# Kernel optimization log

Measured on AMD Instinct MI355X. Metric: run time of the kernel, lower is better.

Reference implementation:

```python
import jax, jax.numpy as jnp
import numpy as np

B, M, N = 32, 2048, 2048
W_PRIMAL, W_DUAL, W_STAT, W_COMP = 0.1, 0.1, 0.6, 0.2


def setup_inputs() -> dict:
    key = jax.random.key(0)
    k1, k2, k3, k4, k5 = jax.random.split(key, 5)
    return {
        "x_hat": jax.random.normal(k1, (B * N,), dtype=jnp.float32),
        "lam_hat": jax.random.normal(k2, (B * M,), dtype=jnp.float32),
        "A": jax.random.normal(k3, (B, M, N), dtype=jnp.float32),
        "b_pad": jax.random.normal(k4, (B, M), dtype=jnp.float32),
        "c_pad": jax.random.normal(k5, (B, N), dtype=jnp.float32),
        "b_mask": jnp.ones((B, M), dtype=bool),
        "c_mask": jnp.ones((B, N), dtype=bool),
    }


def reference(x_hat, lam_hat, A, b_pad, c_pad, b_mask, c_mask):
    # Uniform sizes: x_hat is the concatenation of B vectors of length N,
    # lam_hat of B vectors of length M. b_mask/c_mask are unused by the
    # original forward (full padding assumed here).
    b, m, n = A.shape
    x = x_hat.reshape(b, n)
    lam = lam_hat.reshape(b, m)

    # Batched mat-vec products (the spmm calls in the original, fp32 math).
    Ax_minus_b = jnp.einsum("bmn,bn->bm", A, x) - b_pad        # [B, M]
    At_lambda = jnp.einsum("bmn,bm->bn", A, lam)               # [B, N]

    # Per-sample mean, summed over batch, then * (1/B) == global mean
    # (sizes are uniform).
    loss_primal = jnp.mean(jnp.square(jax.nn.relu(Ax_minus_b)))
    loss_dual = jnp.mean(jnp.square(jax.nn.relu(-lam)))
    loss_stat = jnp.mean(jnp.square(At_lambda + c_pad))
    loss_comp = jnp.mean(jnp.square(lam * Ax_minus_b))

    total = (W_PRIMAL * loss_primal + W_DUAL * loss_dual
             + W_STAT * loss_stat + W_COMP * loss_comp)
    return total
```

## Files before the change

kernel.cpp:

```cpp
#include <hip/hip_runtime.h>

#define BB 32
#define MM 2048
#define NN 2048
#define ROWS 64
#define CHUNKS (MM / ROWS)
#define THREADS 256

typedef float f32x4 __attribute__((ext_vector_type(4)));

#define P0 ((size_t)BB * CHUNKS * NN)
#define P1 (P0 + 2 * BB * CHUNKS)
#define FIN_BLOCKS 64

__device__ __forceinline__ float waveReduceSum(float v) {
#pragma unroll
    for (int off = 32; off > 0; off >>= 1)
        v += __shfl_down(v, off, 64);
    return v;
}

__global__ __launch_bounds__(THREADS) void fused_main(
    const float* __restrict__ x_hat, const float* __restrict__ lam_hat,
    const float* __restrict__ A, const float* __restrict__ b_pad,
    float* __restrict__ ws) {
    const int b = blockIdx.y;
    const int chunk = blockIdx.x;
    const int m0 = chunk * ROWS;
    const int t = threadIdx.x;
    const int wave = t >> 6;
    const int lane = t & 63;

    __shared__ float lamS[ROWS];
    __shared__ float wp[ROWS * 4];

    if (t < ROWS) lamS[t] = lam_hat[b * MM + m0 + t];
    __syncthreads();

    const f32x4* xv = (const f32x4*)(x_hat + (size_t)b * NN);
    const f32x4 x0 = xv[t];
    const f32x4 x1 = xv[256 + t];

    f32x4 at0 = (f32x4)(0.f);
    f32x4 at1 = (f32x4)(0.f);

    const f32x4* Ab = (const f32x4*)(A + ((size_t)b * MM + (size_t)m0) * NN);

    for (int r = 0; r < ROWS; ++r) {
        const f32x4* ap = Ab + (size_t)r * (NN / 4);
        f32x4 a0 = __builtin_nontemporal_load(ap + t);
        f32x4 a1 = __builtin_nontemporal_load(ap + 256 + t);
        float lm = lamS[r];
        f32x4 d = a0 * x0 + a1 * x1;
        float dot = d.x + d.y + d.z + d.w;
        at0 += a0 * lm;
        at1 += a1 * lm;
        float wsum = waveReduceSum(dot);
        if (lane == 0) wp[r * 4 + wave] = wsum;
    }
    __syncthreads();

    if (t < ROWS) {
        int r = t;
        float y = wp[r * 4 + 0] + wp[r * 4 + 1] + wp[r * 4 + 2] + wp[r * 4 + 3]
                - b_pad[b * MM + m0 + r];
        float lm = lamS[r];
        float ry = fmaxf(y, 0.f);
        float pr = ry * ry;
        float cm = lm * y;
        cm = cm * cm;
        pr = waveReduceSum(pr);
        cm = waveReduceSum(cm);
        if (t == 0) {
            float* prcm = ws + P0 + ((size_t)b * CHUNKS + chunk) * 2;
            prcm[0] = pr;
            prcm[1] = cm;
        }
    }

    f32x4* dst = (f32x4*)(ws + ((size_t)b * CHUNKS + chunk) * NN);
    dst[t] = at0;
    dst[256 + t] = at1;
}

__global__ __launch_bounds__(256) void finalize_partial(
    const float* __restrict__ ws_ro, const float* __restrict__ c_pad,
    const float* __restrict__ lam_hat, float* __restrict__ ws) {
    int idx = blockIdx.x * blockDim.x + threadIdx.x;
    int stride = gridDim.x * blockDim.x;
    float stat = 0.f, dual = 0.f, pr = 0.f, cm = 0.f;
    for (int i = idx; i < BB * NN; i += stride) {
        int b = i >> 11;
        int col = i & (NN - 1);
        const float* p = ws_ro + (size_t)b * CHUNKS * NN + col;
        float s = 0.f;
#pragma unroll
        for (int k = 0; k < CHUNKS; ++k) s += p[(size_t)k * NN];
        float v = s + c_pad[i];
        stat += v * v;
        float l = lam_hat[i];
        float rn = fmaxf(-l, 0.f);
        dual += rn * rn;
    }
    for (int i = idx; i < BB * CHUNKS; i += stride) {
        pr += ws_ro[P0 + 2 * i];
        cm += ws_ro[P0 + 2 * i + 1];
    }
    stat = waveReduceSum(stat);
    dual = waveReduceSum(dual);
    pr = waveReduceSum(pr);
    cm = waveReduceSum(cm);
    __shared__ float s[16];
    int wave = threadIdx.x >> 6, lane = threadIdx.x & 63;
    if (lane == 0) {
        s[wave * 4 + 0] = stat; s[wave * 4 + 1] = dual;
        s[wave * 4 + 2] = pr;   s[wave * 4 + 3] = cm;
    }
    __syncthreads();
    if (threadIdx.x < 4) {
        float v = s[threadIdx.x] + s[4 + threadIdx.x] + s[8 + threadIdx.x] + s[12 + threadIdx.x];
        ws[P1 + (size_t)blockIdx.x * 4 + threadIdx.x] = v;
    }
}

__global__ __launch_bounds__(256) void combine_kernel(
    const float* __restrict__ ws_ro, float* __restrict__ out) {
    const int t = threadIdx.x;
    const int wave = t >> 6;
    const int lane = t & 63;
    float v = ws_ro[P1 + (size_t)lane * 4 + wave];
    v = waveReduceSum(v);
    __shared__ float s[4];
    if (lane == 0) s[wave] = v;
    __syncthreads();
    if (t == 0) {
        const float invBM = 1.0f / (float)(BB * MM);
        const float invBN = 1.0f / (float)(BB * NN);
        float stat = s[0] * invBN;
        float dual = s[1] * invBM;
        float primal = s[2] * invBM;
        float comp = s[3] * invBM;
        out[0] = 0.1f * primal + 0.1f * dual + 0.6f * stat + 0.2f * comp;
    }
}

extern "C" void kernel_launch(void* const* d_in, const int* in_sizes, int n_in,
                              void* d_out, int out_size, void* d_ws, size_t ws_size,
                              hipStream_t stream) {
    const float* x_hat   = (const float*)d_in[0];
    const float* lam_hat = (const float*)d_in[1];
    const float* A       = (const float*)d_in[2];
    const float* b_pad   = (const float*)d_in[3];
    const float* c_pad   = (const float*)d_in[4];
    float* out = (float*)d_out;
    float* ws = (float*)d_ws;

    dim3 grid(CHUNKS, BB);
    fused_main<<<grid, THREADS, 0, stream>>>(x_hat, lam_hat, A, b_pad, ws);

    finalize_partial<<<FIN_BLOCKS, 256, 0, stream>>>(ws, c_pad, lam_hat, ws);

    combine_kernel<<<1, 256, 0, stream>>>(ws, out);
}
```

Before: 664.0 us.

## Prefetch next A row, use DPP 16-lane reductions, halve rows per block

The main kernel now software-pipelines the A row loads, issuing the next row's loads before computing on the current one. The per-row 64-lane shuffle reduction is replaced by a 16-lane DPP reduction, with partial sums written to shared memory and combined after the loop. ROWS drops from 64 to 32, which doubles the block count and sets an occupancy hint of 8 blocks per CU. The cost is that the workspace of A^T·lambda partials doubles, so the finalize kernel must read twice as many partials.

New measurement: 951.2 us. 1.43x slower.

```diff
diff --git a/kernel.cpp b/kernel.cpp
--- a/kernel.cpp
+++ b/kernel.cpp
@@ -3,7 +3,7 @@
 #define BB 32
 #define MM 2048
 #define NN 2048
-#define ROWS 64
+#define ROWS 32
 #define CHUNKS (MM / ROWS)
 #define THREADS 256
 
@@ -20,7 +20,22 @@
     return v;
 }
 
-__global__ __launch_bounds__(THREADS) void fused_main(
+template <int CTRL>
+__device__ __forceinline__ float dppAdd(float v) {
+    int s = __builtin_amdgcn_update_dpp(0, __builtin_bit_cast(int, v),
+                                        CTRL, 0xF, 0xF, false);
+    return v + __builtin_bit_cast(float, s);
+}
+
+__device__ __forceinline__ float group16Reduce(float v) {
+    v = dppAdd<0x111>(v);
+    v = dppAdd<0x112>(v);
+    v = dppAdd<0x114>(v);
+    v = dppAdd<0x118>(v);
+    return v;
+}
+
+__global__ __launch_bounds__(THREADS, 8) void fused_main(
     const float* __restrict__ x_hat, const float* __restrict__ lam_hat,
     const float* __restrict__ A, const float* __restrict__ b_pad,
     float* __restrict__ ws) {
@@ -28,11 +43,9 @@
     const int chunk = blockIdx.x;
     const int m0 = chunk * ROWS;
     const int t = threadIdx.x;
-    const int wave = t >> 6;
-    const int lane = t & 63;
 
     __shared__ float lamS[ROWS];
-    __shared__ float wp[ROWS * 4];
+    __shared__ __align__(16) float wp[ROWS * 16];
 
     if (t < ROWS) lamS[t] = lam_hat[b * MM + m0 + t];
     __syncthreads();
@@ -46,29 +59,41 @@
 
     const f32x4* Ab = (const f32x4*)(A + ((size_t)b * MM + (size_t)m0) * NN);
 
+    f32x4 a0 = __builtin_nontemporal_load(Ab + t);
+    f32x4 a1 = __builtin_nontemporal_load(Ab + 256 + t);
+
     for (int r = 0; r < ROWS; ++r) {
-        const f32x4* ap = Ab + (size_t)r * (NN / 4);
-        f32x4 a0 = __builtin_nontemporal_load(ap + t);
-        f32x4 a1 = __builtin_nontemporal_load(ap + 256 + t);
-        float lm = lamS[r];
+        const int rn = (r + 1 < ROWS) ? (r + 1) : r;
+        const f32x4* np = Ab + (size_t)rn * (NN / 4);
+        f32x4 n0 = __builtin_nontemporal_load(np + t);
+        f32x4 n1 = __builtin_nontemporal_load(np + 256 + t);
+
+        const float lm = lamS[r];
         f32x4 d = a0 * x0 + a1 * x1;
-        float dot = d.x + d.y + d.z + d.w;
         at0 += a0 * lm;
         at1 += a1 * lm;
-        float wsum = waveReduceSum(dot);
-        if (lane == 0) wp[r * 4 + wave] = wsum;
+        float dot = (d.x + d.y) + (d.z + d.w);
+        dot = group16Reduce(dot);
+        if ((t & 15) == 15) wp[r * 16 + (t >> 4)] = dot;
+
+        a0 = n0;
+        a1 = n1;
     }
     __syncthreads();
 
-    if (t < ROWS) {
-        int r = t;
-        float y = wp[r * 4 + 0] + wp[r * 4 + 1] + wp[r * 4 + 2] + wp[r * 4 + 3]
-                - b_pad[b * MM + m0 + r];
-        float lm = lamS[r];
-        float ry = fmaxf(y, 0.f);
-        float pr = ry * ry;
-        float cm = lm * y;
-        cm = cm * cm;
+    if (t < 64) {
+        float pr = 0.f, cm = 0.f;
+        if (t < ROWS) {
+            const f32x4* wpv = (const f32x4*)wp;
+            f32x4 s4 = wpv[t * 4 + 0] + wpv[t * 4 + 1] +
+                       wpv[t * 4 + 2] + wpv[t * 4 + 3];
+            float y = (s4.x + s4.y) + (s4.z + s4.w) - b_pad[b * MM + m0 + t];
+            float lm = lamS[t];
+            float ry = fmaxf(y, 0.f);
+            pr = ry * ry;
+            float c = lm * y;
+            cm = c * c;
+        }
         pr = waveReduceSum(pr);
         cm = waveReduceSum(cm);
         if (t == 0) {
@@ -94,7 +119,7 @@
         int col = i & (NN - 1);
         const float* p = ws_ro + (size_t)b * CHUNKS * NN + col;
         float s = 0.f;
-#pragma unroll
+#pragma unroll 16
         for (int k = 0; k < CHUNKS; ++k) s += p[(size_t)k * NN];
         float v = s + c_pad[i];
         stat += v * v;
```
